# Kernel tuning notes

Hardware: AMD Instinct MI355X
Metric: run time of the kernel (lower is better)

## Reference

```python
import jax, jax.numpy as jnp
import numpy as np

N_NODES = 500_000
N_EDGES = 16_000_000
GCN_DIMS = [1, 4, 7, 10, 16]   # gcn layer in/out widths
MLP_DIMS = [16, 32, 16, 16]    # fc1, fc2, fc3 (raw_feature_size=16)


def setup_inputs() -> dict:
    key = jax.random.key(0)
    ks = list(jax.random.split(key, 40))
    ki = iter(ks)
    inp = {}
    inp["x"] = jax.random.normal(next(ki), (N_NODES, 1), dtype=jnp.float32)
    inp["edge_index"] = jax.random.randint(next(ki), (2, N_EDGES), 0, N_NODES, dtype=jnp.int32)
    # GraphConv params: lin_rel (weight+bias) applied to aggregated neighbors,
    # lin_root (weight, no bias) applied to self features.
    for li in range(4):
        din, dout = GCN_DIMS[li], GCN_DIMS[li + 1]
        s = 1.0 / np.sqrt(din)
        inp[f"g{li+1}_Wrel"] = jax.random.uniform(next(ki), (din, dout), jnp.float32, -s, s)
        inp[f"g{li+1}_brel"] = jax.random.uniform(next(ki), (dout,), jnp.float32, -s, s)
        inp[f"g{li+1}_Wroot"] = jax.random.uniform(next(ki), (din, dout), jnp.float32, -s, s)
    for li in range(3):
        din, dout = MLP_DIMS[li], MLP_DIMS[li + 1]
        s = 1.0 / np.sqrt(din)
        inp[f"fc{li+1}_W"] = jax.random.uniform(next(ki), (din, dout), jnp.float32, -s, s)
        inp[f"fc{li+1}_b"] = jax.random.uniform(next(ki), (dout,), jnp.float32, -s, s)
    return inp


def _graph_conv(x, Wrel, brel, Wroot, src, dst):
    # PyG GraphConv, aggr='add': out_i = Wrel @ (sum_{j->i} x_j) + brel + Wroot @ x_i
    agg = jax.ops.segment_sum(x[src], dst, num_segments=N_NODES)  # [N, din]
    return agg @ Wrel + brel + x @ Wroot


def reference(x, edge_index,
              g1_Wrel, g1_brel, g1_Wroot,
              g2_Wrel, g2_brel, g2_Wroot,
              g3_Wrel, g3_brel, g3_Wroot,
              g4_Wrel, g4_brel, g4_Wroot,
              fc1_W, fc1_b, fc2_W, fc2_b, fc3_W, fc3_b):
    src, dst = edge_index[0], edge_index[1]
    h = jax.nn.relu(_graph_conv(x, g1_Wrel, g1_brel, g1_Wroot, src, dst))
    h = jax.nn.relu(_graph_conv(h, g2_Wrel, g2_brel, g2_Wroot, src, dst))
    h = jax.nn.relu(_graph_conv(h, g3_Wrel, g3_brel, g3_Wroot, src, dst))
    h = jax.nn.relu(_graph_conv(h, g4_Wrel, g4_brel, g4_Wroot, src, dst))
    h = jax.nn.relu(h @ fc1_W + fc1_b)
    h = jax.nn.relu(h @ fc2_W + fc2_b)
    return h @ fc3_W + fc3_b
```

## Files before the change

### kernel.cpp

```cpp
#include <hip/hip_runtime.h>
#include <hip/hip_fp16.h>

#define N_NODES 500000
#define N_EDGES 16000000

#define SB_BITS 13
#define SB_SIZE (1 << SB_BITS)
#define NSUPER ((N_NODES + SB_SIZE - 1) / SB_SIZE)
#define CAP1 270336
#define BKT_BITS 9
#define BKT_SIZE (1 << BKT_BITS)
#define NBUCKET ((N_NODES + BKT_SIZE - 1) / BKT_SIZE)
#define BKT_CAP 18432
#define B1_EPT 256
#define B1_CHUNK (256 * B1_EPT)
#define B1_NBLK ((N_EDGES + B1_CHUNK - 1) / B1_CHUNK)
#define B1_VQ (B1_EPT / 4)
#define NV4 (N_EDGES / 4)
#define B2_PER_SUPER 8

__global__ __launch_bounds__(512) void init_bcur_kernel(
    int* __restrict__ bcur1, int* __restrict__ bcur2)
{
    int i = blockIdx.x * 512 + threadIdx.x;
    if (i < NSUPER) bcur1[i] = i * CAP1;
    if (i < NBUCKET) bcur2[i] = i * BKT_CAP;
}

__global__ __launch_bounds__(256) void bin1_kernel(
    const int* __restrict__ src, const int* __restrict__ dst,
    int* __restrict__ bcur1, unsigned int* __restrict__ pairs1)
{
    __shared__ int lh[NSUPER];
    __shared__ int lbase[NSUPER];
    const int4* dst4 = (const int4*)dst;
    const int4* src4 = (const int4*)src;
    int t = threadIdx.x;
    long v0 = (long)blockIdx.x * (B1_CHUNK / 4);

    if (t < NSUPER) lh[t] = 0;
    __syncthreads();

#pragma unroll 8
    for (int q = 0; q < B1_VQ; ++q) {
        long v = v0 + q * 256 + t;
        if (v < NV4) {
            int4 d = dst4[v];
            atomicAdd(&lh[d.x >> SB_BITS], 1);
            atomicAdd(&lh[d.y >> SB_BITS], 1);
            atomicAdd(&lh[d.z >> SB_BITS], 1);
            atomicAdd(&lh[d.w >> SB_BITS], 1);
        }
    }
    __syncthreads();

    if (t < NSUPER) {
        int c = lh[t];
        lbase[t] = c ? atomicAdd(&bcur1[t], c) : 0;
        lh[t] = 0;
    }
    __syncthreads();

#pragma unroll 8
    for (int q = 0; q < B1_VQ; ++q) {
        long v = v0 + q * 256 + t;
        if (v < NV4) {
            int4 d = dst4[v];
            int4 s = src4[v];
            {
                int b = d.x >> SB_BITS;
                int r = atomicAdd(&lh[b], 1);
                pairs1[lbase[b] + r] = ((unsigned int)s.x << SB_BITS) | (unsigned int)(d.x & (SB_SIZE - 1));
            }
            {
                int b = d.y >> SB_BITS;
                int r = atomicAdd(&lh[b], 1);
                pairs1[lbase[b] + r] = ((unsigned int)s.y << SB_BITS) | (unsigned int)(d.y & (SB_SIZE - 1));
            }
            {
                int b = d.z >> SB_BITS;
                int r = atomicAdd(&lh[b], 1);
                pairs1[lbase[b] + r] = ((unsigned int)s.z << SB_BITS) | (unsigned int)(d.z & (SB_SIZE - 1));
            }
            {
                int b = d.w >> SB_BITS;
                int r = atomicAdd(&lh[b], 1);
                pairs1[lbase[b] + r] = ((unsigned int)s.w << SB_BITS) | (unsigned int)(d.w & (SB_SIZE - 1));
            }
        }
    }
}

__global__ __launch_bounds__(256) void bin2_kernel(
    const int* __restrict__ bcur1, int* __restrict__ bcur2,
    const unsigned int* __restrict__ pairs1, unsigned int* __restrict__ pairs2)
{
    __shared__ int lh[16];
    __shared__ int lbase[16];
    int s = blockIdx.x >> 3;
    int blk = blockIdx.x & 7;
    int t = threadIdx.x;
    int count = bcur1[s] - s * CAP1;
    int chunk = (((count + B2_PER_SUPER - 1) / B2_PER_SUPER) + 3) & ~3;
    int lo = blk * chunk;
    int hi = lo + chunk; if (hi > count) hi = count;
    int len = hi > lo ? hi - lo : 0;
    const unsigned int* base = pairs1 + (size_t)s * CAP1 + lo;
    const uint4* p4 = (const uint4*)base;
    int nv = len >> 2;

    if (t < 16) lh[t] = 0;
    __syncthreads();

    for (int i = t; i < nv; i += 256) {
        uint4 p = p4[i];
        atomicAdd(&lh[(p.x & (SB_SIZE - 1)) >> BKT_BITS], 1);
        atomicAdd(&lh[(p.y & (SB_SIZE - 1)) >> BKT_BITS], 1);
        atomicAdd(&lh[(p.z & (SB_SIZE - 1)) >> BKT_BITS], 1);
        atomicAdd(&lh[(p.w & (SB_SIZE - 1)) >> BKT_BITS], 1);
    }
    if (t < (len & 3))
        atomicAdd(&lh[(base[(nv << 2) + t] & (SB_SIZE - 1)) >> BKT_BITS], 1);
    __syncthreads();

    if (t < 16) {
        int c = lh[t];
        lbase[t] = c ? atomicAdd(&bcur2[(s << 4) | t], c) : 0;
        lh[t] = 0;
    }
    __syncthreads();

    for (int i = t; i < nv; i += 256) {
        uint4 p = p4[i];
#pragma unroll
        for (int q = 0; q < 4; ++q) {
            unsigned int e = (q == 0) ? p.x : (q == 1) ? p.y : (q == 2) ? p.z : p.w;
            int sub = (int)((e & (SB_SIZE - 1)) >> BKT_BITS);
            int r = atomicAdd(&lh[sub], 1);
            pairs2[lbase[sub] + r] = ((e >> SB_BITS) << BKT_BITS) | (e & (BKT_SIZE - 1));
        }
    }
    if (t < (len & 3)) {
        unsigned int e = base[(nv << 2) + t];
        int sub = (int)((e & (SB_SIZE - 1)) >> BKT_BITS);
        int r = atomicAdd(&lh[sub], 1);
        pairs2[lbase[sub] + r] = ((e >> SB_BITS) << BKT_BITS) | (e & (BKT_SIZE - 1));
    }
}

__global__ __launch_bounds__(512) void bucket_scan_kernel(
    const int* __restrict__ bcur2, int* __restrict__ bbase)
{
    __shared__ int sdata[512];
    int t = threadIdx.x;
    int i0 = t * 2;
    int v0 = (i0 < NBUCKET) ? (bcur2[i0] - i0 * BKT_CAP) : 0;
    int v1 = (i0 + 1 < NBUCKET) ? (bcur2[i0 + 1] - (i0 + 1) * BKT_CAP) : 0;
    int s = v0 + v1;
    sdata[t] = s;
    __syncthreads();
    for (int o = 1; o < 512; o <<= 1) {
        int tmp = (t >= o) ? sdata[t - o] : 0;
        __syncthreads();
        sdata[t] += tmp;
        __syncthreads();
    }
    int run = sdata[t] - s;
    if (i0 < NBUCKET) bbase[i0] = run;
    if (i0 + 1 < NBUCKET) bbase[i0 + 1] = run + v0;
    if (i0 == NBUCKET - 1) bbase[NBUCKET] = run + v0;
    if (i0 + 1 == NBUCKET - 1) bbase[NBUCKET] = run + v0 + v1;
}

__global__ __launch_bounds__(512) void bucket_sort512_kernel(
    const int* __restrict__ bcur2, const int* __restrict__ bbase,
    const unsigned int* __restrict__ pairs2, const float* __restrict__ xfeat,
    int* __restrict__ off, int* __restrict__ sorted_src,
    float* __restrict__ agg1)
{
    __shared__ int   stage[BKT_CAP];
    __shared__ int   lh[BKT_SIZE];
    __shared__ float laccum[BKT_SIZE];
    __shared__ int   sdata[512];
    int b = blockIdx.x;
    int t = threadIdx.x;
    int base_node = b << BKT_BITS;
    size_t pstart = (size_t)b * BKT_CAP;
    int count = bcur2[b] - b * BKT_CAP;
    int cstart = bbase[b];

    lh[t] = 0; laccum[t] = 0.0f;
    __syncthreads();

    int nv = count >> 2;
    const uint4* p4 = (const uint4*)(pairs2 + pstart);
    for (int i = t; i < nv; i += 512) {
        uint4 p = p4[i];
        atomicAdd(&lh[p.x & (BKT_SIZE - 1)], 1);
        atomicAdd(&lh[p.y & (BKT_SIZE - 1)], 1);
        atomicAdd(&lh[p.z & (BKT_SIZE - 1)], 1);
        atomicAdd(&lh[p.w & (BKT_SIZE - 1)], 1);
    }
    if (t < (count & 3))
        atomicAdd(&lh[pairs2[pstart + (nv << 2) + t] & (BKT_SIZE - 1)], 1);
    __syncthreads();

    int c = lh[t];
    sdata[t] = c;
    __syncthreads();
    for (int o = 1; o < 512; o <<= 1) {
        int tmp = (t >= o) ? sdata[t - o] : 0;
        __syncthreads();
        sdata[t] += tmp;
        __syncthreads();
    }
    int run = cstart + sdata[t] - c;
    int node = base_node + t;
    if (node < N_NODES) {
        off[node] = run;
        if (node == N_NODES - 1) off[N_NODES] = run + c;
    }
    lh[t] = run;
    __syncthreads();

    for (int i = t; i < nv; i += 512) {
        uint4 p = p4[i];
#pragma unroll
        for (int q = 0; q < 4; ++q) {
            unsigned int pe = (q == 0) ? p.x : (q == 1) ? p.y : (q == 2) ? p.z : p.w;
            int low = (int)(pe & (BKT_SIZE - 1));
            int sidx = (int)(pe >> BKT_BITS);
            int pos = atomicAdd(&lh[low], 1);
            stage[pos - cstart] = sidx;
            atomicAdd(&laccum[low], xfeat[sidx]);
        }
    }
    if (t < (count & 3)) {
        unsigned int pe = pairs2[pstart + (nv << 2) + t];
        int low = (int)(pe & (BKT_SIZE - 1));
        int sidx = (int)(pe >> BKT_BITS);
        int pos = atomicAdd(&lh[low], 1);
        stage[pos - cstart] = sidx;
        atomicAdd(&laccum[low], xfeat[sidx]);
    }
    __syncthreads();

    for (int j = t; j < count; j += 512)
        sorted_src[cstart + j] = stage[j];
    if (node < N_NODES) agg1[node] = laccum[t];
}

template<int L>
__global__ __launch_bounds__(256) void gather_h_kernel(
    const int* __restrict__ off, const int* __restrict__ ss,
    const __half2* __restrict__ h, float* __restrict__ agg)
{
    const int npb = 256 / L;
    int node = blockIdx.x * npb + threadIdx.x / L;
    int j = threadIdx.x % L;
    if (node >= N_NODES) return;
    int start = off[node], end = off[node + 1];

    float ax = 0, ay = 0, bx = 0, by = 0, cx = 0, cy = 0, dx = 0, dy = 0;
    int e = start;
    for (; e + 4 <= end; e += 4) {
        int s0 = ss[e], s1 = ss[e + 1], s2 = ss[e + 2], s3 = ss[e + 3];
        __half2 u0 = h[(size_t)s0 * L + j];
        __half2 u1 = h[(size_t)s1 * L + j];
        __half2 u2 = h[(size_t)s2 * L + j];
        __half2 u3 = h[(size_t)s3 * L + j];
        float2 f0 = __half22float2(u0), f1 = __half22float2(u1);
        float2 f2 = __half22float2(u2), f3 = __half22float2(u3);
        ax += f0.x; ay += f0.y;
        bx += f1.x; by += f1.y;
        cx += f2.x; cy += f2.y;
        dx += f3.x; dy += f3.y;
    }
    for (; e < end; ++e) {
        int s0 = ss[e];
        float2 f = __half22float2(h[(size_t)s0 * L + j]);
        ax += f.x; ay += f.y;
    }
    float rx = (ax + bx) + (cx + dx);
    float ry = (ay + by) + (cy + dy);
    ((float2*)agg)[(size_t)node * L + j] = make_float2(rx, ry);
}

__global__ __launch_bounds__(256) void transform1_kernel(
    const float* __restrict__ agg1, const float* __restrict__ x,
    const float* __restrict__ Wrel, const float* __restrict__ brel,
    const float* __restrict__ Wroot,
    __half2* __restrict__ h1)
{
    __shared__ float w[12];
    if (threadIdx.x < 4) {
        w[threadIdx.x] = Wrel[threadIdx.x];
        w[4 + threadIdx.x] = brel[threadIdx.x];
        w[8 + threadIdx.x] = Wroot[threadIdx.x];
    }
    __syncthreads();
    int i = blockIdx.x * blockDim.x + threadIdx.x;
    if (i >= N_NODES) return;
    float a = agg1[i], xv = x[i];
    float r0 = fmaxf(a * w[0] + w[4] + xv * w[8],  0.0f);
    float r1 = fmaxf(a * w[1] + w[5] + xv * w[9],  0.0f);
    float r2 = fmaxf(a * w[2] + w[6] + xv * w[10], 0.0f);
    float r3 = fmaxf(a * w[3] + w[7] + xv * w[11], 0.0f);
    h1[(size_t)i * 2 + 0] = __floats2half2_rn(r0, r1);
    h1[(size_t)i * 2 + 1] = __floats2half2_rn(r2, r3);
}

__global__ __launch_bounds__(256) void transform2_kernel(
    const float* __restrict__ agg, const __half2* __restrict__ h1,
    const float* __restrict__ Wrel, const float* __restrict__ brel,
    const float* __restrict__ Wroot,
    __half2* __restrict__ h2)
{
    __shared__ float sWr[28], sWo[28], sb[7];
    int t = threadIdx.x;
    if (t < 28) { sWr[t] = Wrel[t]; sWo[t] = Wroot[t]; }
    if (t < 7) sb[t] = brel[t];
    __syncthreads();
    int i = blockIdx.x * blockDim.x + threadIdx.x;
    if (i >= N_NODES) return;
    float4 a = ((const float4*)agg)[i];
    float2 x01 = __half22float2(h1[(size_t)i * 2]);
    float2 x23 = __half22float2(h1[(size_t)i * 2 + 1]);
    float av[4] = {a.x, a.y, a.z, a.w};
    float xv[4] = {x01.x, x01.y, x23.x, x23.y};
    float o_[8];
#pragma unroll
    for (int o = 0; o < 7; ++o) {
        float v = sb[o];
#pragma unroll
        for (int k = 0; k < 4; ++k)
            v += av[k] * sWr[k * 7 + o] + xv[k] * sWo[k * 7 + o];
        o_[o] = fmaxf(v, 0.0f);
    }
    o_[7] = 0.0f;
#pragma unroll
    for (int q = 0; q < 4; ++q)
        h2[(size_t)i * 4 + q] = __floats2half2_rn(o_[2 * q], o_[2 * q + 1]);
}

__global__ __launch_bounds__(256) void transform3_kernel(
    const float* __restrict__ agg, const __half2* __restrict__ h2,
    const float* __restrict__ Wrel, const float* __restrict__ brel,
    const float* __restrict__ Wroot,
    __half2* __restrict__ h3)
{
    __shared__ float sWr[70], sWo[70], sb[10];
    int t = threadIdx.x;
    if (t < 70) { sWr[t] = Wrel[t]; sWo[t] = Wroot[t]; }
    if (t < 10) sb[t] = brel[t];
    __syncthreads();
    int i = blockIdx.x * blockDim.x + threadIdx.x;
    if (i >= N_NODES) return;
    const float4* ap = (const float4*)(agg + (size_t)i * 8);
    float4 a0 = ap[0], a1 = ap[1];
    float av[7] = {a0.x, a0.y, a0.z, a0.w, a1.x, a1.y, a1.z};
    float xv[8];
#pragma unroll
    for (int q = 0; q < 4; ++q) {
        float2 f = __half22float2(h2[(size_t)i * 4 + q]);
        xv[2 * q] = f.x; xv[2 * q + 1] = f.y;
    }
    float o_[16];
#pragma unroll
    for (int o = 0; o < 10; ++o) {
        float v = sb[o];
#pragma unroll
        for (int k = 0; k < 7; ++k)
            v += av[k] * sWr[k * 10 + o] + xv[k] * sWo[k * 10 + o];
        o_[o] = fmaxf(v, 0.0f);
    }
#pragma unroll
    for (int o = 10; o < 16; ++o) o_[o] = 0.0f;
#pragma unroll
    for (int q = 0; q < 8; ++q)
        h3[(size_t)i * 8 + q] = __floats2half2_rn(o_[2 * q], o_[2 * q + 1]);
}

__global__ __launch_bounds__(256) void layer4_mlp_kernel(
    const float* __restrict__ agg, const __half2* __restrict__ h3,
    const float* __restrict__ g4Wrel, const float* __restrict__ g4brel,
    const float* __restrict__ g4Wroot,
    const float* __restrict__ fc1W, const float* __restrict__ fc1b,
    const float* __restrict__ fc2W, const float* __restrict__ fc2b,
    const float* __restrict__ fc3W, const float* __restrict__ fc3b,
    float* __restrict__ out)
{
    __shared__ float s[1680];
    float* sWrel  = s;
    float* sbrel  = s + 160;
    float* sWroot = s + 176;
    float* sfc1W  = s + 336;
    float* sfc1b  = s + 848;
    float* sfc2W  = s + 880;
    float* sfc2b  = s + 1392;
    float* sfc3W  = s + 1408;
    float* sfc3b  = s + 1664;
    int t = threadIdx.x;
    for (int i = t; i < 160; i += 256) { sWrel[i] = g4Wrel[i]; sWroot[i] = g4Wroot[i]; }
    for (int i = t; i < 512; i += 256) { sfc1W[i] = fc1W[i]; sfc2W[i] = fc2W[i]; }
    if (t < 256) sfc3W[t] = fc3W[t];
    if (t < 32)  sfc1b[t] = fc1b[t];
    if (t < 16)  { sbrel[t] = g4brel[t]; sfc2b[t] = fc2b[t]; sfc3b[t] = fc3b[t]; }
    __syncthreads();

    int i = blockIdx.x * blockDim.x + threadIdx.x;
    if (i >= N_NODES) return;

    const float4* ap = (const float4*)(agg + (size_t)i * 16);
    float4 a0 = ap[0], a1 = ap[1], a2 = ap[2];
    float a[10] = {a0.x, a0.y, a0.z, a0.w, a1.x, a1.y, a1.z, a1.w, a2.x, a2.y};
    float xin[10];
#pragma unroll
    for (int q = 0; q < 5; ++q) {
        float2 f = __half22float2(h3[(size_t)i * 8 + q]);
        xin[2 * q] = f.x; xin[2 * q + 1] = f.y;
    }

    float h4[16];
#pragma unroll
    for (int o = 0; o < 16; ++o) {
        float v = sbrel[o];
#pragma unroll
        for (int k = 0; k < 10; ++k)
            v += a[k] * sWrel[k * 16 + o] + xin[k] * sWroot[k * 16 + o];
        h4[o] = fmaxf(v, 0.0f);
    }
    float m1[32];
#pragma unroll
    for (int o = 0; o < 32; ++o) {
        float v = sfc1b[o];
#pragma unroll
        for (int k = 0; k < 16; ++k) v += h4[k] * sfc1W[k * 32 + o];
        m1[o] = fmaxf(v, 0.0f);
    }
    float m2[16];
#pragma unroll
    for (int o = 0; o < 16; ++o) {
        float v = sfc2b[o];
#pragma unroll
        for (int k = 0; k < 32; ++k) v += m1[k] * sfc2W[k * 16 + o];
        m2[o] = fmaxf(v, 0.0f);
    }
    float r[16];
#pragma unroll
    for (int o = 0; o < 16; ++o) {
        float v = sfc3b[o];
#pragma unroll
        for (int k = 0; k < 16; ++k) v += m2[k] * sfc3W[k * 16 + o];
        r[o] = v;
    }
    float4* op = (float4*)(out + (size_t)i * 16);
#pragma unroll
    for (int q = 0; q < 4; ++q)
        op[q] = make_float4(r[q * 4 + 0], r[q * 4 + 1], r[q * 4 + 2], r[q * 4 + 3]);
}

extern "C" void kernel_launch(void* const* d_in, const int* in_sizes, int n_in,
                              void* d_out, int out_size, void* d_ws, size_t ws_size,
                              hipStream_t stream) {
    const float* x        = (const float*)d_in[0];
    const int*   ei       = (const int*)d_in[1];
    const float* g1_Wrel  = (const float*)d_in[2];
    const float* g1_brel  = (const float*)d_in[3];
    const float* g1_Wroot = (const float*)d_in[4];
    const float* g2_Wrel  = (const float*)d_in[5];
    const float* g2_brel  = (const float*)d_in[6];
    const float* g2_Wroot = (const float*)d_in[7];
    const float* g3_Wrel  = (const float*)d_in[8];
    const float* g3_brel  = (const float*)d_in[9];
    const float* g3_Wroot = (const float*)d_in[10];
    const float* g4_Wrel  = (const float*)d_in[11];
    const float* g4_brel  = (const float*)d_in[12];
    const float* g4_Wroot = (const float*)d_in[13];
    const float* fc1_W    = (const float*)d_in[14];
    const float* fc1_b    = (const float*)d_in[15];
    const float* fc2_W    = (const float*)d_in[16];
    const float* fc2_b    = (const float*)d_in[17];
    const float* fc3_W    = (const float*)d_in[18];
    const float* fc3_b    = (const float*)d_in[19];
    float* out = (float*)d_out;

    const int* srcp = ei;
    const int* dstp = ei + N_EDGES;

    char* p = (char*)d_ws;
    auto alloc = [&](size_t bytes) {
        char* r = p;
        p += (bytes + 255) & ~(size_t)255;
        return r;
    };
    __half2* h1  = (__half2*)alloc((size_t)N_NODES * 4 * 2);
    __half2* h2  = (__half2*)alloc((size_t)N_NODES * 8 * 2);
    __half2* h3  = (__half2*)alloc((size_t)N_NODES * 16 * 2);
    float*   agg = (float*)  alloc((size_t)N_NODES * 16 * 4);
    alloc((size_t)14 * 1024 * 1024);
    unsigned int* pairs2 = (unsigned int*)h1;
    int* sorted_src = (int*)alloc((size_t)NSUPER * CAP1 * 4);
    unsigned int* pairs1 = (unsigned int*)sorted_src;
    int*   off   = (int*)alloc((size_t)(N_NODES + 1) * 4);
    float* agg1  = (float*)alloc((size_t)N_NODES * 4);
    int*   bcur1 = (int*)alloc((size_t)NSUPER * 4);
    int*   bcur2 = (int*)alloc((size_t)NBUCKET * 4);
    int*   bbase = (int*)alloc((size_t)(NBUCKET + 1) * 4);

    const int TB = 256;
    const int node_blocks = (N_NODES + TB - 1) / TB;

    init_bcur_kernel<<<2, 512, 0, stream>>>(bcur1, bcur2);
    bin1_kernel<<<B1_NBLK, 256, 0, stream>>>(srcp, dstp, bcur1, pairs1);
    bin2_kernel<<<NSUPER * B2_PER_SUPER, 256, 0, stream>>>(bcur1, bcur2, pairs1, pairs2);
    bucket_scan_kernel<<<1, 512, 0, stream>>>(bcur2, bbase);
    bucket_sort512_kernel<<<NBUCKET, 512, 0, stream>>>(
        bcur2, bbase, pairs2, x, off, sorted_src, agg1);

    transform1_kernel<<<node_blocks, TB, 0, stream>>>(
        agg1, x, g1_Wrel, g1_brel, g1_Wroot, h1);

    gather_h_kernel<2><<<(N_NODES + 127) / 128, TB, 0, stream>>>(off, sorted_src, h1, agg);
    transform2_kernel<<<node_blocks, TB, 0, stream>>>(
        agg, h1, g2_Wrel, g2_brel, g2_Wroot, h2);

    gather_h_kernel<4><<<(N_NODES + 63) / 64, TB, 0, stream>>>(off, sorted_src, h2, agg);
    transform3_kernel<<<node_blocks, TB, 0, stream>>>(
        agg, h2, g3_Wrel, g3_brel, g3_Wroot, h3);

    gather_h_kernel<8><<<(N_NODES + 31) / 32, TB, 0, stream>>>(off, sorted_src, h3, agg);
    layer4_mlp_kernel<<<node_blocks, TB, 0, stream>>>(
        agg, h3, g4_Wrel, g4_brel, g4_Wroot,
        fc1_W, fc1_b, fc2_W, fc2_b, fc3_W, fc3_b, out);
}
```

Before: 957.0 us.

## Fuse neighbor gather with per-layer transform through shared-memory tiles

Each CSR gather kernel now writes its aggregated sums into a shared-memory tile and the same block applies the layer transform (and the MLP for the last layer). This removes the float agg round trip through global memory and three kernel launches. The gather loop is unrolled to 8 edges, and output stores use nontemporal hints. The trade-off is that only a fraction of threads do the transform phase, which idles most of the block during the dense stage, and register pressure in the last fused kernel may rise.

```diff
diff --git a/kernel.cpp b/kernel.cpp
--- a/kernel.cpp
+++ b/kernel.cpp
@@ -19,6 +19,12 @@
 #define NV4 (N_EDGES / 4)
 #define B2_PER_SUPER 8
 
+typedef unsigned int u32x2 __attribute__((ext_vector_type(2)));
+typedef unsigned int u32x4 __attribute__((ext_vector_type(4)));
+typedef float f32x4 __attribute__((ext_vector_type(4)));
+
+__device__ __forceinline__ unsigned int h2u(__half2 h) { return *(unsigned int*)&h; }
+
 __global__ __launch_bounds__(512) void init_bcur_kernel(
     int* __restrict__ bcur1, int* __restrict__ bcur2)
 {
@@ -246,44 +252,8 @@
     __syncthreads();
 
     for (int j = t; j < count; j += 512)
-        sorted_src[cstart + j] = stage[j];
-    if (node < N_NODES) agg1[node] = laccum[t];
-}
-
-template<int L>
-__global__ __launch_bounds__(256) void gather_h_kernel(
-    const int* __restrict__ off, const int* __restrict__ ss,
-    const __half2* __restrict__ h, float* __restrict__ agg)
-{
-    const int npb = 256 / L;
-    int node = blockIdx.x * npb + threadIdx.x / L;
-    int j = threadIdx.x % L;
-    if (node >= N_NODES) return;
-    int start = off[node], end = off[node + 1];
-
-    float ax = 0, ay = 0, bx = 0, by = 0, cx = 0, cy = 0, dx = 0, dy = 0;
-    int e = start;
-    for (; e + 4 <= end; e += 4) {
-        int s0 = ss[e], s1 = ss[e + 1], s2 = ss[e + 2], s3 = ss[e + 3];
-        __half2 u0 = h[(size_t)s0 * L + j];
-        __half2 u1 = h[(size_t)s1 * L + j];
-        __half2 u2 = h[(size_t)s2 * L + j];
-        __half2 u3 = h[(size_t)s3 * L + j];
-        float2 f0 = __half22float2(u0), f1 = __half22float2(u1);
-        float2 f2 = __half22float2(u2), f3 = __half22float2(u3);
-        ax += f0.x; ay += f0.y;
-        bx += f1.x; by += f1.y;
-        cx += f2.x; cy += f2.y;
-        dx += f3.x; dy += f3.y;
-    }
-    for (; e < end; ++e) {
-        int s0 = ss[e];
-        float2 f = __half22float2(h[(size_t)s0 * L + j]);
-        ax += f.x; ay += f.y;
-    }
-    float rx = (ax + bx) + (cx + dx);
-    float ry = (ay + by) + (cy + dy);
-    ((float2*)agg)[(size_t)node * L + j] = make_float2(rx, ry);
+        __builtin_nontemporal_store(stage[j], &sorted_src[cstart + j]);
+    if (node < N_NODES) __builtin_nontemporal_store(laccum[t], &agg1[node]);
 }
 
 __global__ __launch_bounds__(256) void transform1_kernel(
@@ -306,83 +276,174 @@
     float r1 = fmaxf(a * w[1] + w[5] + xv * w[9],  0.0f);
     float r2 = fmaxf(a * w[2] + w[6] + xv * w[10], 0.0f);
     float r3 = fmaxf(a * w[3] + w[7] + xv * w[11], 0.0f);
-    h1[(size_t)i * 2 + 0] = __floats2half2_rn(r0, r1);
-    h1[(size_t)i * 2 + 1] = __floats2half2_rn(r2, r3);
-}
-
-__global__ __launch_bounds__(256) void transform2_kernel(
-    const float* __restrict__ agg, const __half2* __restrict__ h1,
+    u32x2 v = { h2u(__floats2half2_rn(r0, r1)), h2u(__floats2half2_rn(r2, r3)) };
+    __builtin_nontemporal_store(v, (u32x2*)(h1 + (size_t)i * 2));
+}
+
+__global__ __launch_bounds__(256) void gather2t_kernel(
+    const int* __restrict__ off, const int* __restrict__ ss,
+    const __half2* __restrict__ h1,
     const float* __restrict__ Wrel, const float* __restrict__ brel,
     const float* __restrict__ Wroot,
     __half2* __restrict__ h2)
 {
+    __shared__ float tile[128 * 5];
     __shared__ float sWr[28], sWo[28], sb[7];
     int t = threadIdx.x;
     if (t < 28) { sWr[t] = Wrel[t]; sWo[t] = Wroot[t]; }
     if (t < 7) sb[t] = brel[t];
-    __syncthreads();
-    int i = blockIdx.x * blockDim.x + threadIdx.x;
-    if (i >= N_NODES) return;
-    float4 a = ((const float4*)agg)[i];
-    float2 x01 = __half22float2(h1[(size_t)i * 2]);
-    float2 x23 = __half22float2(h1[(size_t)i * 2 + 1]);
-    float av[4] = {a.x, a.y, a.z, a.w};
-    float xv[4] = {x01.x, x01.y, x23.x, x23.y};
-    float o_[8];
-#pragma unroll
-    for (int o = 0; o < 7; ++o) {
-        float v = sb[o];
-#pragma unroll
-        for (int k = 0; k < 4; ++k)
-            v += av[k] * sWr[k * 7 + o] + xv[k] * sWo[k * 7 + o];
-        o_[o] = fmaxf(v, 0.0f);
-    }
-    o_[7] = 0.0f;
-#pragma unroll
-    for (int q = 0; q < 4; ++q)
-        h2[(size_t)i * 4 + q] = __floats2half2_rn(o_[2 * q], o_[2 * q + 1]);
-}
-
-__global__ __launch_bounds__(256) void transform3_kernel(
-    const float* __restrict__ agg, const __half2* __restrict__ h2,
+
+    int ln = t >> 1;
+    int j = t & 1;
+    int node = blockIdx.x * 128 + ln;
+    if (node < N_NODES) {
+        int start = off[node], end = off[node + 1];
+        float a0x=0,a0y=0,a1x=0,a1y=0,a2x=0,a2y=0,a3x=0,a3y=0;
+        float b0x=0,b0y=0,b1x=0,b1y=0,b2x=0,b2y=0,b3x=0,b3y=0;
+        int e = start;
+        for (; e + 8 <= end; e += 8) {
+            int s0=ss[e],s1=ss[e+1],s2=ss[e+2],s3=ss[e+3];
+            int s4=ss[e+4],s5=ss[e+5],s6=ss[e+6],s7=ss[e+7];
+            float2 f0=__half22float2(h1[(size_t)s0*2+j]);
+            float2 f1=__half22float2(h1[(size_t)s1*2+j]);
+            float2 f2=__half22float2(h1[(size_t)s2*2+j]);
+            float2 f3=__half22float2(h1[(size_t)s3*2+j]);
+            float2 f4=__half22float2(h1[(size_t)s4*2+j]);
+            float2 f5=__half22float2(h1[(size_t)s5*2+j]);
+            float2 f6=__half22float2(h1[(size_t)s6*2+j]);
+            float2 f7=__half22float2(h1[(size_t)s7*2+j]);
+            a0x+=f0.x;a0y+=f0.y; a1x+=f1.x;a1y+=f1.y;
+            a2x+=f2.x;a2y+=f2.y; a3x+=f3.x;a3y+=f3.y;
+            b0x+=f4.x;b0y+=f4.y; b1x+=f5.x;b1y+=f5.y;
+            b2x+=f6.x;b2y+=f6.y; b3x+=f7.x;b3y+=f7.y;
+        }
+        for (; e < end; ++e) {
+            float2 f = __half22float2(h1[(size_t)ss[e]*2+j]);
+            a0x += f.x; a0y += f.y;
+        }
+        float rx = ((a0x+a1x)+(a2x+a3x)) + ((b0x+b1x)+(b2x+b3x));
+        float ry = ((a0y+a1y)+(a2y+a3y)) + ((b0y+b1y)+(b2y+b3y));
+        tile[ln * 5 + 2 * j] = rx;
+        tile[ln * 5 + 2 * j + 1] = ry;
+    }
+    __syncthreads();
+
+    if (t < 128) {
+        int n2 = blockIdx.x * 128 + t;
+        if (n2 < N_NODES) {
+            float av[4];
+#pragma unroll
+            for (int k = 0; k < 4; ++k) av[k] = tile[t * 5 + k];
+            float2 x01 = __half22float2(h1[(size_t)n2 * 2]);
+            float2 x23 = __half22float2(h1[(size_t)n2 * 2 + 1]);
+            float xv[4] = {x01.x, x01.y, x23.x, x23.y};
+            float o_[8];
+#pragma unroll
+            for (int o = 0; o < 7; ++o) {
+                float v = sb[o];
+#pragma unroll
+                for (int k = 0; k < 4; ++k)
+                    v += av[k] * sWr[k * 7 + o] + xv[k] * sWo[k * 7 + o];
+                o_[o] = fmaxf(v, 0.0f);
+            }
+            o_[7] = 0.0f;
+            u32x4 v = { h2u(__floats2half2_rn(o_[0], o_[1])),
+                        h2u(__floats2half2_rn(o_[2], o_[3])),
+                        h2u(__floats2half2_rn(o_[4], o_[5])),
+                        h2u(__floats2half2_rn(o_[6], o_[7])) };
+            __builtin_nontemporal_store(v, (u32x4*)(h2 + (size_t)n2 * 4));
+        }
+    }
+}
+
+__global__ __launch_bounds__(256) void gather3t_kernel(
+    const int* __restrict__ off, const int* __restrict__ ss,
+    const __half2* __restrict__ h2,
     const float* __restrict__ Wrel, const float* __restrict__ brel,
     const float* __restrict__ Wroot,
     __half2* __restrict__ h3)
 {
+    __shared__ float tile[64 * 9];
     __shared__ float sWr[70], sWo[70], sb[10];
     int t = threadIdx.x;
     if (t < 70) { sWr[t] = Wrel[t]; sWo[t] = Wroot[t]; }
     if (t < 10) sb[t] = brel[t];
-    __syncthreads();
-    int i = blockIdx.x * blockDim.x + threadIdx.x;
-    if (i >= N_NODES) return;
-    const float4* ap = (const float4*)(agg + (size_t)i * 8);
-    float4 a0 = ap[0], a1 = ap[1];
-    float av[7] = {a0.x, a0.y, a0.z, a0.w, a1.x, a1.y, a1.z};
-    float xv[8];
-#pragma unroll
-    for (int q = 0; q < 4; ++q) {
-        float2 f = __half22float2(h2[(size_t)i * 4 + q]);
-        xv[2 * q] = f.x; xv[2 * q + 1] = f.y;
-    }
-    float o_[16];
-#pragma unroll
-    for (int o = 0; o < 10; ++o) {
-        float v = sb[o];
-#pragma unroll
-        for (int k = 0; k < 7; ++k)
-            v += av[k] * sWr[k * 10 + o] + xv[k] * sWo[k * 10 + o];
-        o_[o] = fmaxf(v, 0.0f);
-    }
-#pragma unroll
-    for (int o = 10; o < 16; ++o) o_[o] = 0.0f;
-#pragma unroll
-    for (int q = 0; q < 8; ++q)
-        h3[(size_t)i * 8 + q] = __floats2half2_rn(o_[2 * q], o_[2 * q + 1]);
-}
-
-__global__ __launch_bounds__(256) void layer4_mlp_kernel(
-    const float* __restrict__ agg, const __half2* __restrict__ h3,
+
+    int ln = t >> 2;
+    int j = t & 3;
+    int node = blockIdx.x * 64 + ln;
+    if (node < N_NODES) {
+        int start = off[node], end = off[node + 1];
+        float a0x=0,a0y=0,a1x=0,a1y=0,a2x=0,a2y=0,a3x=0,a3y=0;
+        float b0x=0,b0y=0,b1x=0,b1y=0,b2x=0,b2y=0,b3x=0,b3y=0;
+        int e = start;
+        for (; e + 8 <= end; e += 8) {
+            int s0=ss[e],s1=ss[e+1],s2=ss[e+2],s3=ss[e+3];
+            int s4=ss[e+4],s5=ss[e+5],s6=ss[e+6],s7=ss[e+7];
+            float2 f0=__half22float2(h2[(size_t)s0*4+j]);
+            float2 f1=__half22float2(h2[(size_t)s1*4+j]);
+            float2 f2=__half22float2(h2[(size_t)s2*4+j]);
+            float2 f3=__half22float2(h2[(size_t)s3*4+j]);
+            float2 f4=__half22float2(h2[(size_t)s4*4+j]);
+            float2 f5=__half22float2(h2[(size_t)s5*4+j]);
+            float2 f6=__half22float2(h2[(size_t)s6*4+j]);
+            float2 f7=__half22float2(h2[(size_t)s7*4+j]);
+            a0x+=f0.x;a0y+=f0.y; a1x+=f1.x;a1y+=f1.y;
+            a2x+=f2.x;a2y+=f2.y; a3x+=f3.x;a3y+=f3.y;
+            b0x+=f4.x;b0y+=f4.y; b1x+=f5.x;b1y+=f5.y;
+            b2x+=f6.x;b2y+=f6.y; b3x+=f7.x;b3y+=f7.y;
+        }
+        for (; e < end; ++e) {
+            float2 f = __half22float2(h2[(size_t)ss[e]*4+j]);
+            a0x += f.x; a0y += f.y;
+        }
+        float rx = ((a0x+a1x)+(a2x+a3x)) + ((b0x+b1x)+(b2x+b3x));
+        float ry = ((a0y+a1y)+(a2y+a3y)) + ((b0y+b1y)+(b2y+b3y));
+        tile[ln * 9 + 2 * j] = rx;
+        tile[ln * 9 + 2 * j + 1] = ry;
+    }
+    __syncthreads();
+
+    if (t < 64) {
+        int n2 = blockIdx.x * 64 + t;
+        if (n2 < N_NODES) {
+            float av[7];
+#pragma unroll
+            for (int k = 0; k < 7; ++k) av[k] = tile[t * 9 + k];
+            float xv[8];
+#pragma unroll
+            for (int q = 0; q < 4; ++q) {
+                float2 f = __half22float2(h2[(size_t)n2 * 4 + q]);
+                xv[2 * q] = f.x; xv[2 * q + 1] = f.y;
+            }
+            float o_[16];
+#pragma unroll
+            for (int o = 0; o < 10; ++o) {
+                float v = sb[o];
+#pragma unroll
+                for (int k = 0; k < 7; ++k)
+                    v += av[k] * sWr[k * 10 + o] + xv[k] * sWo[k * 10 + o];
+                o_[o] = fmaxf(v, 0.0f);
+            }
+#pragma unroll
+            for (int o = 10; o < 16; ++o) o_[o] = 0.0f;
+            u32x4 v0 = { h2u(__floats2half2_rn(o_[0], o_[1])),
+                         h2u(__floats2half2_rn(o_[2], o_[3])),
+                         h2u(__floats2half2_rn(o_[4], o_[5])),
+                         h2u(__floats2half2_rn(o_[6], o_[7])) };
+            u32x4 v1 = { h2u(__floats2half2_rn(o_[8], o_[9])),
+                         h2u(__floats2half2_rn(o_[10], o_[11])),
+                         h2u(__floats2half2_rn(o_[12], o_[13])),
+                         h2u(__floats2half2_rn(o_[14], o_[15])) };
+            __builtin_nontemporal_store(v0, (u32x4*)(h3 + (size_t)n2 * 8));
+            __builtin_nontemporal_store(v1, (u32x4*)(h3 + (size_t)n2 * 8 + 4));
+        }
+    }
+}
+
+__global__ __launch_bounds__(256) void gather4t_kernel(
+    const int* __restrict__ off, const int* __restrict__ ss,
+    const __half2* __restrict__ h3,
     const float* __restrict__ g4Wrel, const float* __restrict__ g4brel,
     const float* __restrict__ g4Wroot,
     const float* __restrict__ fc1W, const float* __restrict__ fc1b,
@@ -390,6 +451,7 @@
     const float* __restrict__ fc3W, const float* __restrict__ fc3b,
     float* __restrict__ out)
 {
+    __shared__ float tile[32 * 11];
     __shared__ float s[1680];
     float* sWrel  = s;
     float* sbrel  = s + 160;
@@ -406,58 +468,96 @@
     if (t < 256) sfc3W[t] = fc3W[t];
     if (t < 32)  sfc1b[t] = fc1b[t];
     if (t < 16)  { sbrel[t] = g4brel[t]; sfc2b[t] = fc2b[t]; sfc3b[t] = fc3b[t]; }
-    __syncthreads();
-
-    int i = blockIdx.x * blockDim.x + threadIdx.x;
-    if (i >= N_NODES) return;
-
-    const float4* ap = (const float4*)(agg + (size_t)i * 16);
-    float4 a0 = ap[0], a1 = ap[1], a2 = ap[2];
-    float a[10] = {a0.x, a0.y, a0.z, a0.w, a1.x, a1.y, a1.z, a1.w, a2.x, a2.y};
-    float xin[10];
-#pragma unroll
-    for (int q = 0; q < 5; ++q) {
-        float2 f = __half22float2(h3[(size_t)i * 8 + q]);
-        xin[2 * q] = f.x; xin[2 * q + 1] = f.y;
-    }
-
-    float h4[16];
-#pragma unroll
-    for (int o = 0; o < 16; ++o) {
-        float v = sbrel[o];
-#pragma unroll
-        for (int k = 0; k < 10; ++k)
-            v += a[k] * sWrel[k * 16 + o] + xin[k] * sWroot[k * 16 + o];
-        h4[o] = fmaxf(v, 0.0f);
-    }
-    float m1[32];
-#pragma unroll
-    for (int o = 0; o < 32; ++o) {
-        float v = sfc1b[o];
-#pragma unroll
-        for (int k = 0; k < 16; ++k) v += h4[k] * sfc1W[k * 32 + o];
-        m1[o] = fmaxf(v, 0.0f);
-    }
-    float m2[16];
-#pragma unroll
-    for (int o = 0; o < 16; ++o) {
-        float v = sfc2b[o];
-#pragma unroll
-        for (int k = 0; k < 32; ++k) v += m1[k] * sfc2W[k * 16 + o];
-        m2[o] = fmaxf(v, 0.0f);
-    }
-    float r[16];
-#pragma unroll
-    for (int o = 0; o < 16; ++o) {
-        float v = sfc3b[o];
-#pragma unroll
-        for (int k = 0; k < 16; ++k) v += m2[k] * sfc3W[k * 16 + o];
-        r[o] = v;
-    }
-    float4* op = (float4*)(out + (size_t)i * 16);
-#pragma unroll
-    for (int q = 0; q < 4; ++q)
-        op[q] = make_float4(r[q * 4 + 0], r[q * 4 + 1], r[q * 4 + 2], r[q * 4 + 3]);
+
+    int ln = t >> 3;
+    int j = t & 7;
+    int node = blockIdx.x * 32 + ln;
+    if (node < N_NODES) {
+        int start = off[node], end = off[node + 1];
+        float a0x=0,a0y=0,a1x=0,a1y=0,a2x=0,a2y=0,a3x=0,a3y=0;
+        float b0x=0,b0y=0,b1x=0,b1y=0,b2x=0,b2y=0,b3x=0,b3y=0;
+        int e = start;
+        for (; e + 8 <= end; e += 8) {
+            int s0=ss[e],s1=ss[e+1],s2=ss[e+2],s3=ss[e+3];
+            int s4=ss[e+4],s5=ss[e+5],s6=ss[e+6],s7=ss[e+7];
+            float2 f0=__half22float2(h3[(size_t)s0*8+j]);
+            float2 f1=__half22float2(h3[(size_t)s1*8+j]);
+            float2 f2=__half22float2(h3[(size_t)s2*8+j]);
+            float2 f3=__half22float2(h3[(size_t)s3*8+j]);
+            float2 f4=__half22float2(h3[(size_t)s4*8+j]);
+            float2 f5=__half22float2(h3[(size_t)s5*8+j]);
+            float2 f6=__half22float2(h3[(size_t)s6*8+j]);
+            float2 f7=__half22float2(h3[(size_t)s7*8+j]);
+            a0x+=f0.x;a0y+=f0.y; a1x+=f1.x;a1y+=f1.y;
+            a2x+=f2.x;a2y+=f2.y; a3x+=f3.x;a3y+=f3.y;
+            b0x+=f4.x;b0y+=f4.y; b1x+=f5.x;b1y+=f5.y;
+            b2x+=f6.x;b2y+=f6.y; b3x+=f7.x;b3y+=f7.y;
+        }
+        for (; e < end; ++e) {
+            float2 f = __half22float2(h3[(size_t)ss[e]*8+j]);
+            a0x += f.x; a0y += f.y;
+        }
+        if (j < 5) {
+            float rx = ((a0x+a1x)+(a2x+a3x)) + ((b0x+b1x)+(b2x+b3x));
+            float ry = ((a0y+a1y)+(a2y+a3y)) + ((b0y+b1y)+(b2y+b3y));
+            tile[ln * 11 + 2 * j] = rx;
+            tile[ln * 11 + 2 * j + 1] = ry;
+        }
+    }
+    __syncthreads();
+
+    if (t < 32) {
+        int n2 = blockIdx.x * 32 + t;
+        if (n2 < N_NODES) {
+            float a[10];
+#pragma unroll
+            for (int k = 0; k < 10; ++k) a[k] = tile[t * 11 + k];
+            float xin[10];
+#pragma unroll
+            for (int q = 0; q < 5; ++q) {
+                float2 f = __half22float2(h3[(size_t)n2 * 8 + q]);
+                xin[2 * q] = f.x; xin[2 * q + 1] = f.y;
+            }
+            float h4[16];
+#pragma unroll
+            for (int o = 0; o < 16; ++o) {
+                float v = sbrel[o];
+#pragma unroll
+                for (int k = 0; k < 10; ++k)
+                    v += a[k] * sWrel[k * 16 + o] + xin[k] * sWroot[k * 16 + o];
+                h4[o] = fmaxf(v, 0.0f);
+            }
+            float m1[32];
+#pragma unroll
+            for (int o = 0; o < 32; ++o) {
+                float v = sfc1b[o];
+#pragma unroll
+                for (int k = 0; k < 16; ++k) v += h4[k] * sfc1W[k * 32 + o];
+                m1[o] = fmaxf(v, 0.0f);
+            }
+            float m2[16];
+#pragma unroll
+            for (int o = 0; o < 16; ++o) {
+                float v = sfc2b[o];
+#pragma unroll
+                for (int k = 0; k < 32; ++k) v += m1[k] * sfc2W[k * 16 + o];
+                m2[o] = fmaxf(v, 0.0f);
+            }
+            float r[16];
+#pragma unroll
+            for (int o = 0; o < 16; ++o) {
+                float v = sfc3b[o];
+#pragma unroll
+                for (int k = 0; k < 16; ++k) v += m2[k] * sfc3W[k * 16 + o];
+                r[o] = v;
+            }
+#pragma unroll
+            for (int q = 0; q < 4; ++q) {
+                f32x4 v = { r[q*4+0], r[q*4+1], r[q*4+2], r[q*4+3] };
+                __builtin_nontemporal_store(v, (f32x4*)(out + (size_t)n2 * 16 + q * 4));
+            }
+        }
+    }
 }
 
 extern "C" void kernel_launch(void* const* d_in, const int* in_sizes, int n_in,
@@ -497,8 +597,7 @@
     __half2* h1  = (__half2*)alloc((size_t)N_NODES * 4 * 2);
     __half2* h2  = (__half2*)alloc((size_t)N_NODES * 8 * 2);
     __half2* h3  = (__half2*)alloc((size_t)N_NODES * 16 * 2);
-    float*   agg = (float*)  alloc((size_t)N_NODES * 16 * 4);
-    alloc((size_t)14 * 1024 * 1024);
+    alloc((size_t)46 * 1024 * 1024);
     unsigned int* pairs2 = (unsigned int*)h1;
     int* sorted_src = (int*)alloc((size_t)NSUPER * CAP1 * 4);
     unsigned int* pairs1 = (unsigned int*)sorted_src;
@@ -521,16 +620,11 @@
     transform1_kernel<<<node_blocks, TB, 0, stream>>>(
         agg1, x, g1_Wrel, g1_brel, g1_Wroot, h1);
 
-    gather_h_kernel<2><<<(N_NODES + 127) / 128, TB, 0, stream>>>(off, sorted_src, h1, agg);
-    transform2_kernel<<<node_blocks, TB, 0, stream>>>(
-        agg, h1, g2_Wrel, g2_brel, g2_Wroot, h2);
-
-    gather_h_kernel<4><<<(N_NODES + 63) / 64, TB, 0, stream>>>(off, sorted_src, h2, agg);
-    transform3_kernel<<<node_blocks, TB, 0, stream>>>(
-        agg, h2, g3_Wrel, g3_brel, g3_Wroot, h3);
-
-    gather_h_kernel<8><<<(N_NODES + 31) / 32, TB, 0, stream>>>(off, sorted_src, h3, agg);
-    layer4_mlp_kernel<<<node_blocks, TB, 0, stream>>>(
-        agg, h3, g4_Wrel, g4_brel, g4_Wroot,
+    gather2t_kernel<<<(N_NODES + 127) / 128, TB, 0, stream>>>(
+        off, sorted_src, h1, g2_Wrel, g2_brel, g2_Wroot, h2);
+    gather3t_kernel<<<(N_NODES + 63) / 64, TB, 0, stream>>>(
+        off, sorted_src, h2, g3_Wrel, g3_brel, g3_Wroot, h3);
+    gather4t_kernel<<<(N_NODES + 31) / 32, TB, 0, stream>>>(
+        off, sorted_src, h3, g4_Wrel, g4_brel, g4_Wroot,
         fc1_W, fc1_b, fc2_W, fc2_b, fc3_W, fc3_b, out);
 }
```

Result: slower. 1.087 ms (+13.6%).
